# Kernel optimization log

Hardware: AMD Instinct MI355X
Metric: run time of the kernel (lower is better)

The kernel has to match this reference:

```python
import jax, jax.numpy as jnp
import numpy as np

TEMPERATURE = 0.5


def setup_inputs() -> dict:
    key = jax.random.key(0)
    k1, k2 = jax.random.split(key)
    B, D = 4096, 256
    emb_i = jax.random.normal(k1, (B, D), dtype=jnp.float32)
    emb_j = jax.random.normal(k2, (B, D), dtype=jnp.float32)
    return {"emb_i": emb_i, "emb_j": emb_j}


def reference(emb_i, emb_j):
    B = emb_i.shape[0]
    # L2-normalize along feature dim (torch F.normalize uses eps=1e-12 clamp)
    def l2norm(x):
        n = jnp.sqrt(jnp.sum(x * x, axis=1, keepdims=True))
        return x / jnp.maximum(n, 1e-12)

    z_i = l2norm(emb_i)
    z_j = l2norm(emb_j)
    reps = jnp.concatenate([z_i, z_j], axis=0)  # [2B, D]
    # cosine similarity of normalized rows == plain GEMM
    sim = (reps @ reps.T) / TEMPERATURE  # [2B, 2B]
    # mask out self-similarity on the diagonal
    diag = jnp.eye(2 * B, dtype=bool)
    sim = jnp.where(diag, -jnp.inf, sim)
    # labels: row i -> i+B, row B+i -> i
    labels = jnp.concatenate([jnp.arange(B) + B, jnp.arange(B)])
    logp = jax.nn.log_softmax(sim, axis=1)
    loss = -jnp.mean(jnp.take_along_axis(logp, labels[:, None], axis=1))
    return loss
```

## Files before the change

### kernel.cpp

```cpp
#include <hip/hip_runtime.h>

typedef int i32x4 __attribute__((ext_vector_type(4)));
typedef int i32x8 __attribute__((ext_vector_type(8)));
typedef float f32x4 __attribute__((ext_vector_type(4)));

#define D_DIM 256
#define C2 2.88539008f
#define LN2 0.69314718f

__device__ __forceinline__ int swz(int r) { return ((r & 7) << 1) ^ ((r >> 3) & 1); }

__global__ __launch_bounds__(256) void k_normalize(const float* __restrict__ ei,
                                                   const float* __restrict__ ej,
                                                   unsigned char* __restrict__ R,
                                                   unsigned* __restrict__ ticket,
                                                   int B) {
  if (blockIdx.x == 0 && threadIdx.x == 0) *ticket = 0u;
  const int w = threadIdx.x >> 6, lane = threadIdx.x & 63;
  const int row = blockIdx.x * 16 + w * 4 + (lane >> 4);
  const int kq = lane & 15;
  const float* src = (row < B) ? (ei + (size_t)row * D_DIM)
                               : (ej + (size_t)(row - B) * D_DIM);
  const float4* s4 = (const float4*)src + kq * 4;
  float4 v0 = s4[0], v1 = s4[1], v2 = s4[2], v3 = s4[3];
  float ss = v0.x*v0.x + v0.y*v0.y + v0.z*v0.z + v0.w*v0.w
           + v1.x*v1.x + v1.y*v1.y + v1.z*v1.z + v1.w*v1.w
           + v2.x*v2.x + v2.y*v2.y + v2.z*v2.z + v2.w*v2.w
           + v3.x*v3.x + v3.y*v3.y + v3.z*v3.z + v3.w*v3.w;
#pragma unroll
  for (int d = 1; d < 16; d <<= 1) ss += __shfl_xor(ss, d, 64);
  const float s = 1.0f / fmaxf(sqrtf(ss), 1e-12f);
  int q0 = __builtin_amdgcn_cvt_pk_fp8_f32(v0.x*s, v0.y*s, 0, 0);
  q0     = __builtin_amdgcn_cvt_pk_fp8_f32(v0.z*s, v0.w*s, q0, 1);
  int q1 = __builtin_amdgcn_cvt_pk_fp8_f32(v1.x*s, v1.y*s, 0, 0);
  q1     = __builtin_amdgcn_cvt_pk_fp8_f32(v1.z*s, v1.w*s, q1, 1);
  int q2 = __builtin_amdgcn_cvt_pk_fp8_f32(v2.x*s, v2.y*s, 0, 0);
  q2     = __builtin_amdgcn_cvt_pk_fp8_f32(v2.z*s, v2.w*s, q2, 1);
  int q3 = __builtin_amdgcn_cvt_pk_fp8_f32(v3.x*s, v3.y*s, 0, 0);
  q3     = __builtin_amdgcn_cvt_pk_fp8_f32(v3.z*s, v3.w*s, q3, 1);
  i32x4 o = {q0, q1, q2, q3};
  ((i32x4*)R)[(size_t)row * 16 + kq] = o;
}

__global__ __launch_bounds__(256, 2) void k_simgemm(const unsigned char* __restrict__ R,
                                                    float* __restrict__ rowPartial,
                                                    float* __restrict__ simTgt,
                                                    int N) {
  __shared__ char lds[64 * 1024];
  const int tid = threadIdx.x;
  const int w = tid >> 6, lane = tid & 63;
  const int wr = w >> 1, wc = w & 1;
  const int half = N >> 1;

  const int T = N / 128;
  const int t = blockIdx.x;
  int bi = (int)(((float)(2 * T + 1) -
                  sqrtf((float)((2 * T + 1) * (2 * T + 1) - 8 * t))) * 0.5f);
  while (bi > 0 && t < bi * (2 * T - bi + 1) / 2) --bi;
  while (t >= (bi + 1) * (2 * T - bi) / 2) ++bi;
  const int bj = bi + (t - bi * (2 * T - bi + 1) / 2);
  const int brow = bi * 128, bcol = bj * 128;
  const bool offdiag = (bi != bj);

#pragma unroll
  for (int i = 0; i < 16; ++i) {
    const int cid = i * 256 + tid;
    const int panel = cid >> 11;
    const int pc = cid & 2047;
    const int r = pc >> 4, cs = pc & 15;
    const int c = cs ^ swz(r);
    const unsigned char* g = R + (size_t)((panel ? bcol : brow) + r) * 256 + c * 16;
    __builtin_amdgcn_global_load_lds(
        (const __attribute__((address_space(1))) void*)g,
        (__attribute__((address_space(3))) void*)(lds + (size_t)cid * 16), 16, 0, 0);
  }
  __syncthreads();

  f32x4 zero4 = {0.f, 0.f, 0.f, 0.f};
  f32x4 acc[4][4];
#pragma unroll
  for (int m = 0; m < 4; ++m)
#pragma unroll
    for (int n = 0; n < 4; ++n) acc[m][n] = zero4;

  const char* ldsA = lds;
  const char* ldsB = lds + 32 * 1024;
  auto loadfrag = [&](const char* base, int rl, int ks) -> i32x8 {
    const int g = ks * 4 + (lane >> 4);
    const int s_lo = (2 * g) ^ swz(rl);
    i32x4 lo = *(const i32x4*)(base + rl * 256 + s_lo * 16);
    i32x4 hi = *(const i32x4*)(base + rl * 256 + (s_lo ^ 1) * 16);
    i32x8 f = {lo[0], lo[1], lo[2], lo[3], hi[0], hi[1], hi[2], hi[3]};
    return f;
  };

#pragma unroll
  for (int ks = 0; ks < 2; ++ks) {
    i32x8 a[4], b[4];
#pragma unroll
    for (int m = 0; m < 4; ++m) a[m] = loadfrag(ldsA, wr * 64 + m * 16 + (lane & 15), ks);
#pragma unroll
    for (int n = 0; n < 4; ++n) b[n] = loadfrag(ldsB, wc * 64 + n * 16 + (lane & 15), ks);
#pragma unroll
    for (int m = 0; m < 4; ++m)
#pragma unroll
      for (int n = 0; n < 4; ++n)
        acc[m][n] = __builtin_amdgcn_mfma_scale_f32_16x16x128_f8f6f4(
            a[m], b[n], acc[m][n], 0 , 0 ,
            0, 0x7F7F7F7F , 0, 0x7F7F7F7F );
  }

  float cs4[4] = {0.f, 0.f, 0.f, 0.f};
#pragma unroll
  for (int m = 0; m < 4; ++m) {
#pragma unroll
    for (int j = 0; j < 4; ++j) {
      const int gr = brow + wr * 64 + m * 16 + (lane >> 4) * 4 + j;
      const int tgt = (gr < half) ? gr + half : gr - half;
      float rs = 0.f;
#pragma unroll
      for (int n = 0; n < 4; ++n) {
        const int gc = bcol + wc * 64 + n * 16 + (lane & 15);
        const float sv2 = acc[m][n][j] * C2;
        const float ev = (gr == gc) ? 0.f : __builtin_amdgcn_exp2f(sv2);
        if (gc == tgt) {
          simTgt[gr] = sv2;
          if (offdiag) simTgt[gc] = sv2;
        }
        rs += ev;
        cs4[n] += ev;
      }
#pragma unroll
      for (int d = 1; d < 16; d <<= 1) rs += __shfl_xor(rs, d, 64);
      if ((lane & 15) == 0)
        rowPartial[(size_t)(bj * 2 + wc) * N + gr] = rs;
    }
  }
  if (offdiag) {
#pragma unroll
    for (int n = 0; n < 4; ++n) {
      float c = cs4[n];
      c += __shfl_xor(c, 16, 64);
      c += __shfl_xor(c, 32, 64);
      if ((lane >> 4) == 0)
        rowPartial[(size_t)(bi * 2 + wr) * N + (bcol + wc * 64 + n * 16 + lane)] = c;
    }
  }
}

__global__ __launch_bounds__(256) void k_rowreduce(const float* __restrict__ rowPartial,
                                                   const float* __restrict__ simTgt,
                                                   float* __restrict__ blockOut,
                                                   unsigned* __restrict__ ticket,
                                                   float* __restrict__ out, int N) {
  const int lane = threadIdx.x & 63;
  const int q = threadIdx.x >> 6;
  const int row = blockIdx.x * 64 + lane;
  float part = 0.f;
#pragma unroll 8
  for (int c = q * 32; c < q * 32 + 32; ++c)
    part += rowPartial[(size_t)c * N + row];
  __shared__ float red[4][64];
  __shared__ int isLast;
  red[q][lane] = part;
  __syncthreads();
  if (threadIdx.x < 64) {
    const float denom = red[0][lane] + red[1][lane] + red[2][lane] + red[3][lane];
    float lossr = (__builtin_amdgcn_logf(denom) - simTgt[row]) * LN2;
#pragma unroll
    for (int d = 32; d; d >>= 1) lossr += __shfl_xor(lossr, d, 64);
    if (threadIdx.x == 0) {
      atomicExch(&blockOut[blockIdx.x], lossr);
      isLast = (atomicAdd(ticket, 1u) == gridDim.x - 1);
    }
  }
  __syncthreads();
  if (isLast && threadIdx.x < 64) {
    float v = atomicAdd(&blockOut[threadIdx.x], 0.0f) +
              atomicAdd(&blockOut[64 + threadIdx.x], 0.0f);
#pragma unroll
    for (int d = 32; d; d >>= 1) v += __shfl_xor(v, d, 64);
    if (threadIdx.x == 0) out[0] = v / (float)N;
  }
}

extern "C" void kernel_launch(void* const* d_in, const int* in_sizes, int n_in,
                              void* d_out, int out_size, void* d_ws, size_t ws_size,
                              hipStream_t stream) {
  const float* ei = (const float*)d_in[0];
  const float* ej = (const float*)d_in[1];
  const int B = in_sizes[0] / D_DIM;
  const int N = 2 * B;

  char* ws = (char*)d_ws;
  unsigned char* R = (unsigned char*)ws;
  float* rowPartial = (float*)(ws + (size_t)N * D_DIM);
  float* simTgt     = (float*)(ws + (size_t)N * D_DIM + (size_t)128 * N * 4);
  float* blockOut   = (float*)((char*)simTgt + (size_t)N * 4);
  unsigned* ticket  = (unsigned*)((char*)blockOut + 128 * 4);

  k_normalize<<<N / 16, 256, 0, stream>>>(ei, ej, R, ticket, B);
  const int T = N / 128;
  k_simgemm<<<T * (T + 1) / 2, 256, 0, stream>>>(R, rowPartial, simTgt, N);
  k_rowreduce<<<N / 64, 256, 0, stream>>>(rowPartial, simTgt, blockOut, ticket,
                                          (float*)d_out, N);
}
```

Baseline: 51.84 us.

## Make sim GEMM persistent with double-buffered LDS prefetch and packed partials

The sim GEMM becomes a persistent kernel of 256 blocks with 512 threads. Each block loops over upper-triangular tiles and prefetches the next tile into a second LDS buffer while computing the current one. The rowPartial layout is packed per row block so only valid partials are stored, and the row reduce reads just those entries. The aim is to overlap global-to-LDS loads with MFMA and exp work and to cut the launch tail and wasted reduce traffic. The cost is 128KB of LDS per block with one block per CU, plus hardcoded constants (12352, 257, 256) that assume T=64.

```diff
diff --git a/kernel.cpp b/kernel.cpp
--- a/kernel.cpp
+++ b/kernel.cpp
@@ -9,6 +9,15 @@
 #define LN2 0.69314718f
 
 __device__ __forceinline__ int swz(int r) { return ((r & 7) << 1) ^ ((r >> 3) & 1); }
+
+__device__ __forceinline__ void decode(int t, int T, int& bi, int& bj) {
+  int b = (int)(((float)(2 * T + 1) -
+                 sqrtf((float)((2 * T + 1) * (2 * T + 1) - 8 * t))) * 0.5f);
+  while (b > 0 && t < b * (2 * T - b + 1) / 2) --b;
+  while (t >= (b + 1) * (2 * T - b) / 2) ++b;
+  bi = b;
+  bj = b + (t - b * (2 * T - b + 1) / 2);
+}
 
 __global__ __launch_bounds__(256) void k_normalize(const float* __restrict__ ei,
                                                    const float* __restrict__ ej,
@@ -42,49 +51,33 @@
   ((i32x4*)R)[(size_t)row * 16 + kq] = o;
 }
 
-__global__ __launch_bounds__(256, 2) void k_simgemm(const unsigned char* __restrict__ R,
+__global__ __launch_bounds__(512, 1) void k_simgemm(const unsigned char* __restrict__ R,
                                                     float* __restrict__ rowPartial,
                                                     float* __restrict__ simTgt,
-                                                    int N) {
-  __shared__ char lds[64 * 1024];
+                                                    int N, int NT) {
+  __shared__ char lds[2][64 * 1024];
   const int tid = threadIdx.x;
   const int w = tid >> 6, lane = tid & 63;
-  const int wr = w >> 1, wc = w & 1;
-  const int half = N >> 1;
-
-  const int T = N / 128;
-  const int t = blockIdx.x;
-  int bi = (int)(((float)(2 * T + 1) -
-                  sqrtf((float)((2 * T + 1) * (2 * T + 1) - 8 * t))) * 0.5f);
-  while (bi > 0 && t < bi * (2 * T - bi + 1) / 2) --bi;
-  while (t >= (bi + 1) * (2 * T - bi) / 2) ++bi;
-  const int bj = bi + (t - bi * (2 * T - bi + 1) / 2);
-  const int brow = bi * 128, bcol = bj * 128;
-  const bool offdiag = (bi != bj);
-
-#pragma unroll
-  for (int i = 0; i < 16; ++i) {
-    const int cid = i * 256 + tid;
-    const int panel = cid >> 11;
-    const int pc = cid & 2047;
-    const int r = pc >> 4, cs = pc & 15;
-    const int c = cs ^ swz(r);
-    const unsigned char* g = R + (size_t)((panel ? bcol : brow) + r) * 256 + c * 16;
-    __builtin_amdgcn_global_load_lds(
-        (const __attribute__((address_space(1))) void*)g,
-        (__attribute__((address_space(3))) void*)(lds + (size_t)cid * 16), 16, 0, 0);
-  }
-  __syncthreads();
-
-  f32x4 zero4 = {0.f, 0.f, 0.f, 0.f};
-  f32x4 acc[4][4];
-#pragma unroll
-  for (int m = 0; m < 4; ++m)
-#pragma unroll
-    for (int n = 0; n < 4; ++n) acc[m][n] = zero4;
-
-  const char* ldsA = lds;
-  const char* ldsB = lds + 32 * 1024;
+  const int wr = w >> 2, wc = w & 3;
+  const int half = N >> 1, T = N / 128;
+
+  auto stage = [&](int buf, int sbi, int sbj) {
+    char* dst = lds[buf];
+#pragma unroll
+    for (int i = 0; i < 8; ++i) {
+      const int cid = i * 512 + tid;
+      const int panel = cid >> 11;
+      const int pc = cid & 2047;
+      const int r = pc >> 4, cs = pc & 15;
+      const int c = cs ^ swz(r);
+      const unsigned char* g =
+          R + (size_t)((panel ? sbj : sbi) * 128 + r) * 256 + c * 16;
+      __builtin_amdgcn_global_load_lds(
+          (const __attribute__((address_space(1))) void*)g,
+          (__attribute__((address_space(3))) void*)(dst + (size_t)cid * 16), 16, 0, 0);
+    }
+  };
+
   auto loadfrag = [&](const char* base, int rl, int ks) -> i32x8 {
     const int g = ks * 4 + (lane >> 4);
     const int s_lo = (2 * g) ^ swz(rl);
@@ -94,57 +87,96 @@
     return f;
   };
 
-#pragma unroll
-  for (int ks = 0; ks < 2; ++ks) {
-    i32x8 a[4], b[4];
-#pragma unroll
-    for (int m = 0; m < 4; ++m) a[m] = loadfrag(ldsA, wr * 64 + m * 16 + (lane & 15), ks);
-#pragma unroll
-    for (int n = 0; n < 4; ++n) b[n] = loadfrag(ldsB, wc * 64 + n * 16 + (lane & 15), ks);
+  int bi, bj;
+  if ((int)blockIdx.x < NT) decode(blockIdx.x, T, bi, bj);
+  else return;
+  stage(0, bi, bj);
+  int cur = 0;
+
+  for (int t = blockIdx.x; t < NT; t += 256) {
+    const int brow = bi * 128, bcol = bj * 128;
+    const bool offdiag = (bi != bj);
+    int nbi = 0, nbj = 0;
+    const bool hasNext = (t + 256 < NT);
+    if (hasNext) {
+      decode(t + 256, T, nbi, nbj);
+      stage(cur ^ 1, nbi, nbj);
+      asm volatile("s_waitcnt vmcnt(8)" ::: "memory");
+    } else {
+      asm volatile("s_waitcnt vmcnt(0)" ::: "memory");
+    }
+    __builtin_amdgcn_s_barrier();
+
+    f32x4 acc[4][2];
 #pragma unroll
     for (int m = 0; m < 4; ++m)
 #pragma unroll
-      for (int n = 0; n < 4; ++n)
-        acc[m][n] = __builtin_amdgcn_mfma_scale_f32_16x16x128_f8f6f4(
-            a[m], b[n], acc[m][n], 0 , 0 ,
-            0, 0x7F7F7F7F , 0, 0x7F7F7F7F );
-  }
-
-  float cs4[4] = {0.f, 0.f, 0.f, 0.f};
-#pragma unroll
-  for (int m = 0; m < 4; ++m) {
-#pragma unroll
-    for (int j = 0; j < 4; ++j) {
-      const int gr = brow + wr * 64 + m * 16 + (lane >> 4) * 4 + j;
-      const int tgt = (gr < half) ? gr + half : gr - half;
-      float rs = 0.f;
-#pragma unroll
-      for (int n = 0; n < 4; ++n) {
-        const int gc = bcol + wc * 64 + n * 16 + (lane & 15);
-        const float sv2 = acc[m][n][j] * C2;
-        const float ev = (gr == gc) ? 0.f : __builtin_amdgcn_exp2f(sv2);
-        if (gc == tgt) {
-          simTgt[gr] = sv2;
-          if (offdiag) simTgt[gc] = sv2;
+      for (int n = 0; n < 2; ++n) acc[m][n] = (f32x4){0.f, 0.f, 0.f, 0.f};
+
+    const char* ldsA = lds[cur];
+    const char* ldsB = lds[cur] + 32 * 1024;
+#pragma unroll
+    for (int ks = 0; ks < 2; ++ks) {
+      i32x8 a[4], b[2];
+#pragma unroll
+      for (int m = 0; m < 4; ++m)
+        a[m] = loadfrag(ldsA, wr * 64 + m * 16 + (lane & 15), ks);
+#pragma unroll
+      for (int n = 0; n < 2; ++n)
+        b[n] = loadfrag(ldsB, wc * 32 + n * 16 + (lane & 15), ks);
+#pragma unroll
+      for (int m = 0; m < 4; ++m)
+#pragma unroll
+        for (int n = 0; n < 2; ++n)
+          acc[m][n] = __builtin_amdgcn_mfma_scale_f32_16x16x128_f8f6f4(
+              a[m], b[n], acc[m][n], 0 , 0 ,
+              0, 0x7F7F7F7F, 0, 0x7F7F7F7F);
+    }
+
+    const int rbaseA = (257 * bi - bi * bi) * 128;
+    const int rbaseB = (257 * bj - bj * bj) * 128;
+    float cs4[2] = {0.f, 0.f};
+#pragma unroll
+    for (int m = 0; m < 4; ++m) {
+#pragma unroll
+      for (int j = 0; j < 4; ++j) {
+        const int gr = brow + wr * 64 + m * 16 + (lane >> 4) * 4 + j;
+        const int tgt = (gr < half) ? gr + half : gr - half;
+        float rs = 0.f;
+#pragma unroll
+        for (int n = 0; n < 2; ++n) {
+          const int gc = bcol + wc * 32 + n * 16 + (lane & 15);
+          const float sv2 = acc[m][n][j] * C2;
+          const float ev = (gr == gc) ? 0.f : __builtin_amdgcn_exp2f(sv2);
+          if (gc == tgt) {
+            simTgt[gr] = sv2;
+            if (offdiag) simTgt[gc] = sv2;
+          }
+          rs += ev;
+          cs4[n] += ev;
         }
-        rs += ev;
-        cs4[n] += ev;
+#pragma unroll
+        for (int d = 1; d < 16; d <<= 1) rs += __shfl_xor(rs, d, 64);
+        if ((lane & 15) == 0)
+          rowPartial[rbaseA + (4 * (bj - bi) + wc) * 128 + (gr & 127)] = rs;
       }
-#pragma unroll
-      for (int d = 1; d < 16; d <<= 1) rs += __shfl_xor(rs, d, 64);
-      if ((lane & 15) == 0)
-        rowPartial[(size_t)(bj * 2 + wc) * N + gr] = rs;
-    }
-  }
-  if (offdiag) {
-#pragma unroll
-    for (int n = 0; n < 4; ++n) {
-      float c = cs4[n];
-      c += __shfl_xor(c, 16, 64);
-      c += __shfl_xor(c, 32, 64);
-      if ((lane >> 4) == 0)
-        rowPartial[(size_t)(bi * 2 + wr) * N + (bcol + wc * 64 + n * 16 + lane)] = c;
-    }
+    }
+    if (offdiag) {
+#pragma unroll
+      for (int n = 0; n < 2; ++n) {
+        float c = cs4[n];
+        c += __shfl_xor(c, 16, 64);
+        c += __shfl_xor(c, 32, 64);
+        if (lane < 16)
+          rowPartial[rbaseB + (4 * (T - bj) + 2 * bi + wr) * 128 +
+                     (wc * 32 + n * 16 + lane)] = c;
+      }
+    }
+
+    asm volatile("s_waitcnt lgkmcnt(0)" ::: "memory");
+    __builtin_amdgcn_s_barrier();
+    cur ^= 1;
+    bi = nbi; bj = nbj;
   }
 }
 
@@ -156,10 +188,12 @@
   const int lane = threadIdx.x & 63;
   const int q = threadIdx.x >> 6;
   const int row = blockIdx.x * 64 + lane;
+  const int b = row >> 7;
+  const int cnt = 256 - 2 * b;
+  const int base = (257 * b - b * b) * 128;
+  const int lr = row & 127;
   float part = 0.f;
-#pragma unroll 8
-  for (int c = q * 32; c < q * 32 + 32; ++c)
-    part += rowPartial[(size_t)c * N + row];
+  for (int s = q; s < cnt; s += 4) part += rowPartial[base + s * 128 + lr];
   __shared__ float red[4][64];
   __shared__ int isLast;
   red[q][lane] = part;
@@ -191,17 +225,18 @@
   const float* ej = (const float*)d_in[1];
   const int B = in_sizes[0] / D_DIM;
   const int N = 2 * B;
+  const int T = N / 128;
+  const int NT = T * (T + 1) / 2;
 
   char* ws = (char*)d_ws;
   unsigned char* R = (unsigned char*)ws;
   float* rowPartial = (float*)(ws + (size_t)N * D_DIM);
-  float* simTgt     = (float*)(ws + (size_t)N * D_DIM + (size_t)128 * N * 4);
+  float* simTgt     = (float*)((char*)rowPartial + (size_t)12352 * 128 * 4);
   float* blockOut   = (float*)((char*)simTgt + (size_t)N * 4);
   unsigned* ticket  = (unsigned*)((char*)blockOut + 128 * 4);
 
   k_normalize<<<N / 16, 256, 0, stream>>>(ei, ej, R, ticket, B);
-  const int T = N / 128;
-  k_simgemm<<<T * (T + 1) / 2, 256, 0, stream>>>(R, rowPartial, simTgt, N);
+  k_simgemm<<<256, 512, 0, stream>>>(R, rowPartial, simTgt, N, NT);
   k_rowreduce<<<N / 64, 256, 0, stream>>>(rowPartial, simTgt, blockOut, ticket,
                                           (float*)d_out, N);
 }
```

Measured after the change: 79.42 us. 53.2% more time.

## Double-buffer K-sliced LDS staging with 16x16x32 fp8 MFMA for higher occupancy

Applied to the files above, without the earlier changes.

Replaces the one-shot load of full 128x256 fp8 panels into 64KB of LDS with a double-buffered loop over eight K slices of 32 bytes, using 16KB of LDS total. Launch bounds rise from 2 to 5 blocks per CU so global loads can overlap compute across blocks and iterations. The scaled 16x16x128 f8f6f4 MFMA is swapped for the plain 16x16x32 fp8 MFMA, so the kernel issues four times as many MFMA instructions and two barriers per slice. The swizzle is dropped, which may bring LDS bank conflicts on the 32-byte-stride rows.

```diff
diff --git a/kernel.cpp b/kernel.cpp
--- a/kernel.cpp
+++ b/kernel.cpp
@@ -1,14 +1,11 @@
 #include <hip/hip_runtime.h>
 
 typedef int i32x4 __attribute__((ext_vector_type(4)));
-typedef int i32x8 __attribute__((ext_vector_type(8)));
 typedef float f32x4 __attribute__((ext_vector_type(4)));
 
 #define D_DIM 256
 #define C2 2.88539008f
 #define LN2 0.69314718f
-
-__device__ __forceinline__ int swz(int r) { return ((r & 7) << 1) ^ ((r >> 3) & 1); }
 
 __global__ __launch_bounds__(256) void k_normalize(const float* __restrict__ ei,
                                                    const float* __restrict__ ej,
@@ -42,11 +39,11 @@
   ((i32x4*)R)[(size_t)row * 16 + kq] = o;
 }
 
-__global__ __launch_bounds__(256, 2) void k_simgemm(const unsigned char* __restrict__ R,
+__global__ __launch_bounds__(256, 5) void k_simgemm(const unsigned char* __restrict__ R,
                                                     float* __restrict__ rowPartial,
                                                     float* __restrict__ simTgt,
                                                     int N) {
-  __shared__ char lds[64 * 1024];
+  __shared__ char lds[2][8 * 1024];
   const int tid = threadIdx.x;
   const int w = tid >> 6, lane = tid & 63;
   const int wr = w >> 1, wc = w & 1;
@@ -62,52 +59,63 @@
   const int brow = bi * 128, bcol = bj * 128;
   const bool offdiag = (bi != bj);
 
-#pragma unroll
-  for (int i = 0; i < 16; ++i) {
-    const int cid = i * 256 + tid;
-    const int panel = cid >> 11;
-    const int pc = cid & 2047;
-    const int r = pc >> 4, cs = pc & 15;
-    const int c = cs ^ swz(r);
-    const unsigned char* g = R + (size_t)((panel ? bcol : brow) + r) * 256 + c * 16;
-    __builtin_amdgcn_global_load_lds(
-        (const __attribute__((address_space(1))) void*)g,
-        (__attribute__((address_space(3))) void*)(lds + (size_t)cid * 16), 16, 0, 0);
-  }
-  __syncthreads();
-
-  f32x4 zero4 = {0.f, 0.f, 0.f, 0.f};
   f32x4 acc[4][4];
 #pragma unroll
   for (int m = 0; m < 4; ++m)
 #pragma unroll
-    for (int n = 0; n < 4; ++n) acc[m][n] = zero4;
-
-  const char* ldsA = lds;
-  const char* ldsB = lds + 32 * 1024;
-  auto loadfrag = [&](const char* base, int rl, int ks) -> i32x8 {
-    const int g = ks * 4 + (lane >> 4);
-    const int s_lo = (2 * g) ^ swz(rl);
-    i32x4 lo = *(const i32x4*)(base + rl * 256 + s_lo * 16);
-    i32x4 hi = *(const i32x4*)(base + rl * 256 + (s_lo ^ 1) * 16);
-    i32x8 f = {lo[0], lo[1], lo[2], lo[3], hi[0], hi[1], hi[2], hi[3]};
-    return f;
+    for (int n = 0; n < 4; ++n) acc[m][n] = (f32x4){0.f, 0.f, 0.f, 0.f};
+
+  auto stage = [&](int buf, int kt) {
+    char* dst = lds[buf];
+#pragma unroll
+    for (int i = 0; i < 2; ++i) {
+      const int cid = i * 256 + tid;
+      const int panel = cid >> 8;
+      const int pc = cid & 255;
+      const int r = pc >> 1, c = pc & 1;
+      const unsigned char* g =
+          R + (size_t)((panel ? bcol : brow) + r) * 256 + kt * 32 + c * 16;
+      __builtin_amdgcn_global_load_lds(
+          (const __attribute__((address_space(1))) void*)g,
+          (__attribute__((address_space(3))) void*)(dst + (size_t)cid * 16), 16, 0, 0);
+    }
   };
 
-#pragma unroll
-  for (int ks = 0; ks < 2; ++ks) {
-    i32x8 a[4], b[4];
-#pragma unroll
-    for (int m = 0; m < 4; ++m) a[m] = loadfrag(ldsA, wr * 64 + m * 16 + (lane & 15), ks);
-#pragma unroll
-    for (int n = 0; n < 4; ++n) b[n] = loadfrag(ldsB, wc * 64 + n * 16 + (lane & 15), ks);
+  auto compute = [&](int buf) {
+    const char* ldsA = lds[buf];
+    const char* ldsB = lds[buf] + 4 * 1024;
+    const int g = lane >> 4;
+    long a[4], b[4];
+#pragma unroll
+    for (int m = 0; m < 4; ++m) {
+      const int row = wr * 64 + m * 16 + (lane & 15);
+      a[m] = *(const long*)(ldsA + row * 32 + g * 8);
+    }
+#pragma unroll
+    for (int n = 0; n < 4; ++n) {
+      const int col = wc * 64 + n * 16 + (lane & 15);
+      b[n] = *(const long*)(ldsB + col * 32 + g * 8);
+    }
 #pragma unroll
     for (int m = 0; m < 4; ++m)
 #pragma unroll
       for (int n = 0; n < 4; ++n)
-        acc[m][n] = __builtin_amdgcn_mfma_scale_f32_16x16x128_f8f6f4(
-            a[m], b[n], acc[m][n], 0 , 0 ,
-            0, 0x7F7F7F7F , 0, 0x7F7F7F7F );
+        acc[m][n] = __builtin_amdgcn_mfma_f32_16x16x32_fp8_fp8(a[m], b[n], acc[m][n], 0, 0, 0);
+  };
+
+  stage(0, 0);
+#pragma unroll
+  for (int kt = 0; kt < 8; ++kt) {
+    const int cur = kt & 1;
+    if (kt < 7) {
+      stage(cur ^ 1, kt + 1);
+      asm volatile("s_waitcnt vmcnt(2)" ::: "memory");
+    } else {
+      asm volatile("s_waitcnt vmcnt(0)" ::: "memory");
+    }
+    __builtin_amdgcn_s_barrier();
+    compute(cur);
+    __builtin_amdgcn_s_barrier();
   }
 
   float cs4[4] = {0.f, 0.f, 0.f, 0.f};
```

New measurement: 65.10 us. 25.6% more time.

## Pre-pack FP8 operands in MFMA fragment layout and load directly to registers

Applied to the files above, without the earlier changes.

The normalize kernel now writes the FP8 matrix in a tiled layout matching the MFMA operand fragment order. The GEMM kernel then drops the 64 KB LDS staging and loads each lane's 8-byte fragments straight from global memory into registers. It also switches from the scaled 16x16x128 MFMA to the 16x16x32 fp8 MFMA over eight k-steps. This removes the LDS round trip and barrier and may improve occupancy, but issues many small 8-byte global loads and runs more, smaller MFMA instructions.

```diff
diff --git a/kernel.cpp b/kernel.cpp
--- a/kernel.cpp
+++ b/kernel.cpp
@@ -1,14 +1,12 @@
 #include <hip/hip_runtime.h>
 
 typedef int i32x4 __attribute__((ext_vector_type(4)));
-typedef int i32x8 __attribute__((ext_vector_type(8)));
 typedef float f32x4 __attribute__((ext_vector_type(4)));
 
 #define D_DIM 256
 #define C2 2.88539008f
 #define LN2 0.69314718f
 
-__device__ __forceinline__ int swz(int r) { return ((r & 7) << 1) ^ ((r >> 3) & 1); }
 
 __global__ __launch_bounds__(256) void k_normalize(const float* __restrict__ ei,
                                                    const float* __restrict__ ej,
@@ -39,17 +37,19 @@
   int q3 = __builtin_amdgcn_cvt_pk_fp8_f32(v3.x*s, v3.y*s, 0, 0);
   q3     = __builtin_amdgcn_cvt_pk_fp8_f32(v3.z*s, v3.w*s, q3, 1);
   i32x4 o = {q0, q1, q2, q3};
-  ((i32x4*)R)[(size_t)row * 16 + kq] = o;
+  const size_t idx = (((size_t)(row >> 4) * 8 + (kq >> 1)) * 16 + (row & 15)) * 32
+                   + (size_t)(kq & 1) * 16;
+  *(i32x4*)(R + idx) = o;
 }
 
 __global__ __launch_bounds__(256, 2) void k_simgemm(const unsigned char* __restrict__ R,
                                                     float* __restrict__ rowPartial,
                                                     float* __restrict__ simTgt,
                                                     int N) {
-  __shared__ char lds[64 * 1024];
   const int tid = threadIdx.x;
   const int w = tid >> 6, lane = tid & 63;
   const int wr = w >> 1, wc = w & 1;
+  const int c15 = lane & 15, g = lane >> 4;
   const int half = N >> 1;
 
   const int T = N / 128;
@@ -62,65 +62,49 @@
   const int brow = bi * 128, bcol = bj * 128;
   const bool offdiag = (bi != bj);
 
+  const size_t laneOff = (size_t)c15 * 32 + (size_t)g * 8;
+  const char* Ab = (const char*)R + ((size_t)(brow >> 4) + wr * 4) * 4096 + laneOff;
+  const char* Bb = (const char*)R + ((size_t)(bcol >> 4) + wc * 4) * 4096 + laneOff;
+  long a[4][8], b[4][8];
 #pragma unroll
-  for (int i = 0; i < 16; ++i) {
-    const int cid = i * 256 + tid;
-    const int panel = cid >> 11;
-    const int pc = cid & 2047;
-    const int r = pc >> 4, cs = pc & 15;
-    const int c = cs ^ swz(r);
-    const unsigned char* g = R + (size_t)((panel ? bcol : brow) + r) * 256 + c * 16;
-    __builtin_amdgcn_global_load_lds(
-        (const __attribute__((address_space(1))) void*)g,
-        (__attribute__((address_space(3))) void*)(lds + (size_t)cid * 16), 16, 0, 0);
-  }
-  __syncthreads();
+  for (int m = 0; m < 4; ++m)
+#pragma unroll
+    for (int kt = 0; kt < 8; ++kt)
+      a[m][kt] = *(const long*)(Ab + (size_t)m * 4096 + (size_t)kt * 512);
+#pragma unroll
+  for (int n = 0; n < 4; ++n)
+#pragma unroll
+    for (int kt = 0; kt < 8; ++kt)
+      b[n][kt] = *(const long*)(Bb + (size_t)n * 4096 + (size_t)kt * 512);
 
-  f32x4 zero4 = {0.f, 0.f, 0.f, 0.f};
+  asm volatile("s_waitcnt vmcnt(0)" ::: "memory");
+  __builtin_amdgcn_sched_barrier(0);
+
   f32x4 acc[4][4];
 #pragma unroll
   for (int m = 0; m < 4; ++m)
 #pragma unroll
-    for (int n = 0; n < 4; ++n) acc[m][n] = zero4;
-
-  const char* ldsA = lds;
-  const char* ldsB = lds + 32 * 1024;
-  auto loadfrag = [&](const char* base, int rl, int ks) -> i32x8 {
-    const int g = ks * 4 + (lane >> 4);
-    const int s_lo = (2 * g) ^ swz(rl);
-    i32x4 lo = *(const i32x4*)(base + rl * 256 + s_lo * 16);
-    i32x4 hi = *(const i32x4*)(base + rl * 256 + (s_lo ^ 1) * 16);
-    i32x8 f = {lo[0], lo[1], lo[2], lo[3], hi[0], hi[1], hi[2], hi[3]};
-    return f;
-  };
-
+    for (int n = 0; n < 4; ++n) acc[m][n] = (f32x4){0.f, 0.f, 0.f, 0.f};
 #pragma unroll
-  for (int ks = 0; ks < 2; ++ks) {
-    i32x8 a[4], b[4];
-#pragma unroll
-    for (int m = 0; m < 4; ++m) a[m] = loadfrag(ldsA, wr * 64 + m * 16 + (lane & 15), ks);
-#pragma unroll
-    for (int n = 0; n < 4; ++n) b[n] = loadfrag(ldsB, wc * 64 + n * 16 + (lane & 15), ks);
+  for (int kt = 0; kt < 8; ++kt)
 #pragma unroll
     for (int m = 0; m < 4; ++m)
 #pragma unroll
       for (int n = 0; n < 4; ++n)
-        acc[m][n] = __builtin_amdgcn_mfma_scale_f32_16x16x128_f8f6f4(
-            a[m], b[n], acc[m][n], 0 , 0 ,
-            0, 0x7F7F7F7F , 0, 0x7F7F7F7F );
-  }
+        acc[m][n] = __builtin_amdgcn_mfma_f32_16x16x32_fp8_fp8(
+            a[m][kt], b[n][kt], acc[m][n], 0, 0, 0);
 
   float cs4[4] = {0.f, 0.f, 0.f, 0.f};
 #pragma unroll
   for (int m = 0; m < 4; ++m) {
 #pragma unroll
     for (int j = 0; j < 4; ++j) {
-      const int gr = brow + wr * 64 + m * 16 + (lane >> 4) * 4 + j;
+      const int gr = brow + wr * 64 + m * 16 + g * 4 + j;
       const int tgt = (gr < half) ? gr + half : gr - half;
       float rs = 0.f;
 #pragma unroll
       for (int n = 0; n < 4; ++n) {
-        const int gc = bcol + wc * 64 + n * 16 + (lane & 15);
+        const int gc = bcol + wc * 64 + n * 16 + c15;
         const float sv2 = acc[m][n][j] * C2;
         const float ev = (gr == gc) ? 0.f : __builtin_amdgcn_exp2f(sv2);
         if (gc == tgt) {
@@ -132,7 +116,7 @@
       }
 #pragma unroll
       for (int d = 1; d < 16; d <<= 1) rs += __shfl_xor(rs, d, 64);
-      if ((lane & 15) == 0)
+      if (c15 == 0)
         rowPartial[(size_t)(bj * 2 + wc) * N + gr] = rs;
     }
   }
@@ -142,8 +126,8 @@
       float c = cs4[n];
       c += __shfl_xor(c, 16, 64);
       c += __shfl_xor(c, 32, 64);
-      if ((lane >> 4) == 0)
-        rowPartial[(size_t)(bi * 2 + wr) * N + (bcol + wc * 64 + n * 16 + lane)] = c;
+      if (g == 0)
+        rowPartial[(size_t)(bi * 2 + wr) * N + (bcol + wc * 64 + n * 16 + c15)] = c;
     }
   }
 }
```

After: 59.49 us. 1.15x slower.
